# Kernel optimization log

Hardware: AMD Instinct MI355X
Metric: run time of the kernel (lower is better)

The kernel has to match this reference:

```python
import jax, jax.numpy as jnp
import numpy as np

NEG_SLOPE = 0.2  # PyG GATConv default negative_slope


def gat_conv(x, src, dst, W, a_src, a_dst, b, n_nodes):
    # x: [N, Cin]; W: [H, Cin, Cout]; a_src/a_dst: [H, Cout]; b: [Cout]
    xh = jnp.einsum('ni,hio->nho', x, W)                 # [N, H, Cout]
    al_s = jnp.einsum('nho,ho->nh', xh, a_src)           # [N, H]
    al_d = jnp.einsum('nho,ho->nh', xh, a_dst)           # [N, H]
    e = jax.nn.leaky_relu(al_s[src] + al_d[dst], NEG_SLOPE)  # [E, H]
    # softmax over incoming edges of each dst node (self-loops guarantee >=1 edge)
    m = jax.ops.segment_max(e, dst, num_segments=n_nodes)
    ex = jnp.exp(e - m[dst])
    den = jax.ops.segment_sum(ex, dst, num_segments=n_nodes)
    alpha = ex / den[dst]                                # [E, H]
    msg = alpha[:, :, None] * xh[src]                    # [E, H, Cout]
    out = jax.ops.segment_sum(msg, dst, num_segments=n_nodes)  # [N, H, Cout]
    return out.mean(axis=1) + b                          # concat=False -> head mean


def setup_inputs() -> dict:
    key = jax.random.key(0)
    ks = jax.random.split(key, 16)
    N, E, C, H = 20000, 320000, 128, 4
    s = 1.0 / np.sqrt(C)
    inp = {
        'x': jax.random.normal(ks[0], (N, C), dtype=jnp.float32),
        'edge_index': jax.random.randint(ks[1], (2, E), 0, N, dtype=jnp.int64),
    }
    for i, name in enumerate(['1', '2', 'r']):
        k0, k1, k2 = jax.random.split(ks[2 + i], 3)
        inp['W' + name] = jax.random.normal(k0, (H, C, C), dtype=jnp.float32) * s
        inp['as' + name] = jax.random.normal(k1, (H, C), dtype=jnp.float32) * s
        inp['ad' + name] = jax.random.normal(k2, (H, C), dtype=jnp.float32) * s
        inp['b' + name] = jnp.zeros((C,), dtype=jnp.float32)
    return inp


def reference(x, edge_index, W1, as1, ad1, b1, W2, as2, ad2, b2, Wr, asr, adr, br):
    n = x.shape[0]
    loop = jnp.arange(n, dtype=edge_index.dtype)
    src = jnp.concatenate([edge_index[0], loop])  # PyG add_self_loops=True
    dst = jnp.concatenate([edge_index[1], loop])
    h = gat_conv(x, src, dst, W1, as1, ad1, b1, n)
    h = gat_conv(h, src, dst, W2, as2, ad2, b2, n)
    res = gat_conv(x, src, dst, Wr, asr, adr, br, n)
    return h + res
```

## Files before the change

### kernel.cpp

```cpp
#include <hip/hip_runtime.h>
#include <math.h>

#define C 128

typedef unsigned short u16;
typedef __attribute__((ext_vector_type(8))) short short8;
typedef __attribute__((ext_vector_type(4))) float f32x4;
typedef __attribute__((ext_vector_type(4))) u16 u16x4;

__device__ __forceinline__ float b2f(u16 u) {
    union { unsigned i; float f; } x; x.i = (unsigned)u << 16; return x.f;
}
__device__ __forceinline__ u16 f2b(float f) {
    union { float f; unsigned i; } x; x.f = f;
    unsigned r = x.i + 0x7FFFu + ((x.i >> 16) & 1u);
    return (u16)(r >> 16);
}
__device__ __forceinline__ float lrelu(float x) { return x > 0.f ? x : 0.2f * x; }


__global__ void hist_kernel(const int* __restrict__ ei, int E, int N,
                            int* __restrict__ count) {
    int total = E + N;
    for (int e = blockIdx.x * blockDim.x + threadIdx.x; e < total;
         e += gridDim.x * blockDim.x) {
        int d = (e < E) ? ei[E + e] : (e - E);
        if ((unsigned)d < (unsigned)N) atomicAdd(&count[d], 1);
    }
}

__global__ __launch_bounds__(1024) void scan_kernel(const int* __restrict__ count,
                                                    int* __restrict__ offs,
                                                    int* __restrict__ cursor, int N) {
    int tid = threadIdx.x, lane = tid & 63, wid = tid >> 6;
    int CH = (N + 1023) >> 10;
    int base = tid * CH;
    int s = 0;
    for (int j = 0; j < CH; ++j) {
        int i = base + j;
        if (i < N) s += count[i];
    }
    int own = s;
    #pragma unroll
    for (int d = 1; d < 64; d <<= 1) {
        int v = __shfl_up(s, d);
        if (lane >= d) s += v;
    }
    __shared__ int wtot[16];
    if (lane == 63) wtot[wid] = s;
    __syncthreads();
    if (tid < 16) {
        int t = wtot[tid];
        int u = t;
        #pragma unroll
        for (int d = 1; d < 16; d <<= 1) {
            int v = __shfl_up(u, d);
            if (tid >= d) u += v;
        }
        wtot[tid] = u - t;
        if (tid == 15) offs[N] = u;
    }
    __syncthreads();
    int run = wtot[wid] + s - own;
    for (int j = 0; j < CH; ++j) {
        int i = base + j;
        if (i < N) {
            offs[i] = run;
            cursor[i] = run;
            run += count[i];
        }
    }
}

__global__ void scatter_kernel(const int* __restrict__ ei, int E, int N,
                               int* __restrict__ cursor, int* __restrict__ srcs,
                               int* __restrict__ dsts) {
    int total = E + N;
    for (int e = blockIdx.x * blockDim.x + threadIdx.x; e < total;
         e += gridDim.x * blockDim.x) {
        int sNode, d;
        if (e < E) { sNode = ei[e]; d = ei[E + e]; }
        else       { sNode = e - E; d = sNode; }
        if ((unsigned)d < (unsigned)N && (unsigned)sNode < (unsigned)N) {
            int pos = atomicAdd(&cursor[d], 1);
            srcs[pos] = sNode;
            dsts[pos] = d;
        }
    }
}


__global__ __launch_bounds__(256) void cvt_w_kernel(const float* __restrict__ W1,
                                                    const float* __restrict__ Wr,
                                                    const float* __restrict__ W2,
                                                    u16* __restrict__ Wf) {
    int idx = blockIdx.x * 256 + threadIdx.x;
    int lane = idx & 63;
    int kk = (idx >> 6) & 15;
    int t = (idx >> 10) & 7;
    int l = idx >> 13;
    if (l >= 3) return;
    const float* W = (l == 0) ? W1 : (l == 1) ? Wr : W2;
    int o = t * 16 + (lane & 15);
    int bk = kk * 32 + (lane >> 4) * 8;
    int h = bk >> 7, i0 = bk & 127;
    short8 v;
    #pragma unroll
    for (int j = 0; j < 8; ++j) {
        v[j] = (short)f2b(0.25f * W[((size_t)h * C + i0 + j) * C + o]);
    }
    *(short8*)(Wf + (size_t)idx * 8) = v;
}


__global__ __launch_bounds__(256) void wvec_kernel(const float* __restrict__ W1,
                                                   const float* __restrict__ as1,
                                                   const float* __restrict__ ad1,
                                                   const float* __restrict__ Wr,
                                                   const float* __restrict__ asr,
                                                   const float* __restrict__ adr,
                                                   const float* __restrict__ W2,
                                                   const float* __restrict__ as2,
                                                   const float* __restrict__ ad2,
                                                   u16* __restrict__ vsdA,
                                                   u16* __restrict__ vsdB) {
    int slot = blockIdx.x;
    const float* W  = (slot < 4) ? W1 : (slot < 8) ? Wr : W2;
    const float* s_ = (slot < 4) ? as1 : (slot < 8) ? asr : as2;
    const float* d_ = (slot < 4) ? ad1 : (slot < 8) ? adr : ad2;
    int h = slot & 3;
    int wave = threadIdx.x >> 6, lane = threadIdx.x & 63;
    int rbase = blockIdx.y * 32 + wave * 8;
    float as0 = s_[h * C + lane], as1v = s_[h * C + 64 + lane];
    float ad0 = d_[h * C + lane], ad1v = d_[h * C + 64 + lane];
    #pragma unroll
    for (int j = 0; j < 8; ++j) {
        int i = rbase + j;
        const float* Wrow = W + ((size_t)h * C + i) * C;
        float w0 = Wrow[lane], w1 = Wrow[64 + lane];
        float ps = w0 * as0 + w1 * as1v;
        float pd = w0 * ad0 + w1 * ad1v;
        #pragma unroll
        for (int m = 32; m; m >>= 1) {
            ps += __shfl_xor(ps, m);
            pd += __shfl_xor(pd, m);
        }
        if (lane == 0) {
            if (slot < 8) {
                vsdA[slot * C + i] = f2b(ps);
                vsdA[(8 + slot) * C + i] = f2b(pd);
            } else {
                vsdB[(slot - 8) * C + i] = f2b(ps);
                vsdB[(4 + (slot - 8)) * C + i] = f2b(pd);
            }
        }
    }
}


__global__ __launch_bounds__(256) void alA_kernel(const float* __restrict__ x,
                                                  const u16* __restrict__ vsd,
                                                  u16* __restrict__ xb,
                                                  float* __restrict__ als,
                                                  float* __restrict__ ald, int N) {
    int wave = threadIdx.x >> 6, lane = threadIdx.x & 63;
    int rowBase = blockIdx.x * 64 + wave * 16;
    int r = rowBase + (lane & 15);
    int rl = r < N ? r : N - 1;
    int kg = (lane >> 4) * 8;

    short8 a[4];
    #pragma unroll
    for (int t = 0; t < 4; ++t) {
        const float* xp = x + (size_t)rl * C + t * 32 + kg;
        float4 f0 = *(const float4*)xp;
        float4 f1 = *(const float4*)(xp + 4);
        short8 s;
        s[0] = f2b(f0.x); s[1] = f2b(f0.y); s[2] = f2b(f0.z); s[3] = f2b(f0.w);
        s[4] = f2b(f1.x); s[5] = f2b(f1.y); s[6] = f2b(f1.z); s[7] = f2b(f1.w);
        a[t] = s;
        if (r < N) *(short8*)(xb + (size_t)r * C + t * 32 + kg) = s;
    }
    f32x4 acc = {0.f, 0.f, 0.f, 0.f};
    int col = lane & 15;
    #pragma unroll
    for (int t = 0; t < 4; ++t) {
        short8 b = *(const short8*)(vsd + (size_t)col * C + t * 32 + kg);
        acc = __builtin_amdgcn_mfma_f32_16x16x32_bf16(a[t], b, acc, 0, 0, 0);
    }
    #pragma unroll
    for (int j = 0; j < 4; ++j) {
        int rr = rowBase + (lane >> 4) * 4 + j;
        if (rr < N) {
            if (col < 8) als[rr * 8 + col] = acc[j];
            else ald[rr * 8 + (col - 8)] = acc[j];
        }
    }
}


__global__ __launch_bounds__(256) void alB_kernel(const u16* __restrict__ in,
                                                  const u16* __restrict__ vsd,
                                                  float* __restrict__ als,
                                                  float* __restrict__ ald, int N) {
    int wave = threadIdx.x >> 6, lane = threadIdx.x & 63;
    int rowBase = blockIdx.x * 64 + wave * 16;
    int r = rowBase + (lane & 15);
    int rl = r < N ? r : N - 1;
    int kg = (lane >> 4) * 8;

    f32x4 acc = {0.f, 0.f, 0.f, 0.f};
    int col = lane & 15;
    #pragma unroll
    for (int t = 0; t < 4; ++t) {
        short8 a = *(const short8*)(in + (size_t)rl * C + t * 32 + kg);
        short8 b = *(const short8*)(vsd + (size_t)col * C + t * 32 + kg);
        acc = __builtin_amdgcn_mfma_f32_16x16x32_bf16(a, b, acc, 0, 0, 0);
    }
    #pragma unroll
    for (int j = 0; j < 4; ++j) {
        int rr = rowBase + (lane >> 4) * 4 + j;
        if (rr < N && col < 8) {
            if (col < 4) als[rr * 4 + col] = acc[j];
            else ald[rr * 4 + (col - 4)] = acc[j];
        }
    }
}


template <int NH>
__global__ __launch_bounds__(256) void ew_kernel(const float* __restrict__ als,
                                                 const float* __restrict__ ald,
                                                 const int* __restrict__ srcs,
                                                 const int* __restrict__ dsts,
                                                 float* __restrict__ wout, int ET) {
    int i = blockIdx.x * blockDim.x + threadIdx.x;
    if (i >= ET) return;
    int s = srcs[i], d = dsts[i];
    const float* as_ = als + (size_t)s * NH;
    const float* ad_ = ald + (size_t)d * NH;
    float* wo = wout + (size_t)i * NH;
    #pragma unroll
    for (int h = 0; h < NH; ++h) {
        wo[h] = __expf(lrelu(as_[h] + ad_[h]));
    }
}


template <int NH>
__global__ __launch_bounds__(256) void den_kernel(const float* __restrict__ wgt,
                                                  const int* __restrict__ offs,
                                                  float* __restrict__ den, int N) {
    int idx = blockIdx.x * blockDim.x + threadIdx.x;
    int node = idx / NH, h = idx % NH;
    if (node >= N) return;
    int beg = offs[node], end = offs[node + 1];
    float s = 0.f;
    for (int i = beg; i < end; ++i) s += wgt[(size_t)i * NH + h];
    den[idx] = s;
}


template <int NH>
__global__ __launch_bounds__(256) void aggx_kernel(const u16* __restrict__ xsrc,
                                                   const float* __restrict__ wgt,
                                                   const float* __restrict__ den,
                                                   const int* __restrict__ offs,
                                                   const int* __restrict__ srcs,
                                                   u16* __restrict__ dest, int N) {
    constexpr int NHG = NH / 2;
    int node = blockIdx.x * 4 + (threadIdx.x >> 6);
    int lane = threadIdx.x & 63;
    if (node >= N) return;
    int g = lane >> 5;
    int c0 = (lane & 31) * 4;
    int beg = offs[node], end = offs[node + 1];

    float inv[NHG];
    #pragma unroll
    for (int j = 0; j < NHG; ++j) {
        inv[j] = 1.f / den[(size_t)node * NH + g * NHG + j];
    }

    float acc[NHG][4] = {};
    int i = beg;
    for (; i + 8 <= end; i += 8) {
        int s[8];
        #pragma unroll
        for (int e = 0; e < 8; ++e) s[e] = srcs[i + e];
        u16x4 v[8];
        #pragma unroll
        for (int e = 0; e < 8; ++e) {
            v[e] = *(const u16x4*)(xsrc + (size_t)s[e] * C + c0);
        }
        float wv[8][NHG];
        #pragma unroll
        for (int e = 0; e < 8; ++e) {
            if constexpr (NHG == 4) {
                float4 wq = *(const float4*)(wgt + (size_t)(i + e) * NH + g * NHG);
                wv[e][0] = wq.x; wv[e][1] = wq.y; wv[e][2] = wq.z; wv[e][3] = wq.w;
            } else {
                float2 wq = *(const float2*)(wgt + (size_t)(i + e) * NH + g * NHG);
                wv[e][0] = wq.x; wv[e][1] = wq.y;
            }
        }
        #pragma unroll
        for (int e = 0; e < 8; ++e) {
            float f[4];
            #pragma unroll
            for (int j = 0; j < 4; ++j) f[j] = b2f(v[e][j]);
            #pragma unroll
            for (int j2 = 0; j2 < NHG; ++j2) {
                #pragma unroll
                for (int j = 0; j < 4; ++j) acc[j2][j] += wv[e][j2] * f[j];
            }
        }
    }
    for (; i < end; ++i) {
        int s0 = srcs[i];
        u16x4 v0 = *(const u16x4*)(xsrc + (size_t)s0 * C + c0);
        float w0[NHG];
        #pragma unroll
        for (int j2 = 0; j2 < NHG; ++j2) {
            w0[j2] = wgt[(size_t)i * NH + g * NHG + j2];
        }
        float f[4];
        #pragma unroll
        for (int j = 0; j < 4; ++j) f[j] = b2f(v0[j]);
        #pragma unroll
        for (int j2 = 0; j2 < NHG; ++j2) {
            #pragma unroll
            for (int j = 0; j < 4; ++j) acc[j2][j] += w0[j2] * f[j];
        }
    }

    #pragma unroll
    for (int j2 = 0; j2 < NHG; ++j2) {
        int h = g * NHG + j2;
        u16x4 o = {f2b(acc[j2][0] * inv[j2]), f2b(acc[j2][1] * inv[j2]),
                   f2b(acc[j2][2] * inv[j2]), f2b(acc[j2][3] * inv[j2])};
        *(u16x4*)(dest + (size_t)node * (NH * C) + h * C + c0) = o;
    }
}


__global__ __launch_bounds__(256) void gemm2ab_kernel(const u16* __restrict__ agg,
                                                      const u16* __restrict__ Wf,
                                                      const float* __restrict__ b1,
                                                      const float* __restrict__ br,
                                                      u16* __restrict__ h1b,
                                                      float* __restrict__ outf, int N) {
    int part = blockIdx.y;
    const float* bias = part ? br : b1;
    int wave = threadIdx.x >> 6, lane = threadIdx.x & 63;
    int rowBase = blockIdx.x * 128 + wave * 32;
    int p = lane & 15, q = lane >> 4;
    int r0 = rowBase + p, r1 = rowBase + 16 + p;
    int rl0 = r0 < N ? r0 : N - 1;
    int rl1 = r1 < N ? r1 : N - 1;
    int kg = q * 8;

    const short8* ap0 = (const short8*)(agg + (size_t)rl0 * 1024 + part * 512 + kg);
    const short8* ap1 = (const short8*)(agg + (size_t)rl1 * 1024 + part * 512 + kg);
    const u16* wb = Wf + (size_t)part * 65536 + lane * 8;

    f32x4 acc0[8], acc1[8];
    #pragma unroll
    for (int t = 0; t < 8; ++t) {
        acc0[t] = (f32x4){0.f, 0.f, 0.f, 0.f};
        acc1[t] = (f32x4){0.f, 0.f, 0.f, 0.f};
    }

    #pragma unroll
    for (int kk = 0; kk < 16; ++kk) {
        short8 a0 = ap0[kk * 4];
        short8 a1 = ap1[kk * 4];
        #pragma unroll
        for (int t = 0; t < 8; ++t) {
            short8 b = *(const short8*)(wb + (size_t)(t * 16 + kk) * 512);
            acc0[t] = __builtin_amdgcn_mfma_f32_16x16x32_bf16(a0, b, acc0[t], 0, 0, 0);
            acc1[t] = __builtin_amdgcn_mfma_f32_16x16x32_bf16(a1, b, acc1[t], 0, 0, 0);
        }
    }

    #pragma unroll
    for (int t = 0; t < 8; ++t) {
        int col = t * 16 + p;
        float bcol = bias[col];
        #pragma unroll
        for (int j = 0; j < 4; ++j) {
            int rr0 = rowBase + q * 4 + j;
            int rr1 = rowBase + 16 + q * 4 + j;
            if (rr0 < N) {
                float v = acc0[t][j] + bcol;
                if (part == 0) h1b[(size_t)rr0 * C + col] = f2b(v);
                else outf[(size_t)rr0 * C + col] = v;
            }
            if (rr1 < N) {
                float v = acc1[t][j] + bcol;
                if (part == 0) h1b[(size_t)rr1 * C + col] = f2b(v);
                else outf[(size_t)rr1 * C + col] = v;
            }
        }
    }
}


__global__ __launch_bounds__(256) void gemm2c_kernel(const u16* __restrict__ A,
                                                     const u16* __restrict__ Wf,
                                                     const float* __restrict__ bias,
                                                     float* __restrict__ outf, int N) {
    int wave = threadIdx.x >> 6, lane = threadIdx.x & 63;
    int rowBase = blockIdx.x * 128 + wave * 32;
    int p = lane & 15, q = lane >> 4;
    int r0 = rowBase + p, r1 = rowBase + 16 + p;
    int rl0 = r0 < N ? r0 : N - 1;
    int rl1 = r1 < N ? r1 : N - 1;
    int kg = q * 8;

    const short8* ap0 = (const short8*)(A + (size_t)rl0 * 512 + kg);
    const short8* ap1 = (const short8*)(A + (size_t)rl1 * 512 + kg);
    const u16* wb = Wf + (size_t)2 * 65536 + lane * 8;

    f32x4 acc0[8], acc1[8];
    #pragma unroll
    for (int t = 0; t < 8; ++t) {
        acc0[t] = (f32x4){0.f, 0.f, 0.f, 0.f};
        acc1[t] = (f32x4){0.f, 0.f, 0.f, 0.f};
    }

    #pragma unroll
    for (int kk = 0; kk < 16; ++kk) {
        short8 a0 = ap0[kk * 4];
        short8 a1 = ap1[kk * 4];
        #pragma unroll
        for (int t = 0; t < 8; ++t) {
            short8 b = *(const short8*)(wb + (size_t)(t * 16 + kk) * 512);
            acc0[t] = __builtin_amdgcn_mfma_f32_16x16x32_bf16(a0, b, acc0[t], 0, 0, 0);
            acc1[t] = __builtin_amdgcn_mfma_f32_16x16x32_bf16(a1, b, acc1[t], 0, 0, 0);
        }
    }

    #pragma unroll
    for (int t = 0; t < 8; ++t) {
        int col = t * 16 + p;
        float bcol = bias[col];
        #pragma unroll
        for (int j = 0; j < 4; ++j) {
            int rr0 = rowBase + q * 4 + j;
            int rr1 = rowBase + 16 + q * 4 + j;
            if (rr0 < N) outf[(size_t)rr0 * C + col] += acc0[t][j] + bcol;
            if (rr1 < N) outf[(size_t)rr1 * C + col] += acc1[t][j] + bcol;
        }
    }
}


extern "C" void kernel_launch(void* const* d_in, const int* in_sizes, int n_in,
                              void* d_out, int out_size, void* d_ws, size_t ws_size,
                              hipStream_t stream) {
    const float* x = (const float*)d_in[0];
    const int* ei = (const int*)d_in[1];
    const float* W1 = (const float*)d_in[2];
    const float* as1 = (const float*)d_in[3];
    const float* ad1 = (const float*)d_in[4];
    const float* b1 = (const float*)d_in[5];
    const float* W2 = (const float*)d_in[6];
    const float* as2 = (const float*)d_in[7];
    const float* ad2 = (const float*)d_in[8];
    const float* b2 = (const float*)d_in[9];
    const float* Wr = (const float*)d_in[10];
    const float* asr = (const float*)d_in[11];
    const float* adr = (const float*)d_in[12];
    const float* br = (const float*)d_in[13];

    int N = in_sizes[0] / C;
    int E = in_sizes[1] / 2;
    int ET = E + N;

    size_t sz_xb    = (size_t)N * C * 2;
    size_t sz_h1b   = (size_t)N * C * 2;
    size_t sz_aggA  = (size_t)N * 1024 * 2;
    size_t sz_aggB  = (size_t)N * 512 * 2;
    size_t sz_wc    = (size_t)3 * C * 512 * 2;
    size_t sz_vsd   = (size_t)16 * C * 2;
    size_t sz_al8   = (size_t)N * 8 * 4;
    size_t sz_count = (size_t)N * 4;
    size_t sz_den8  = (size_t)N * 8 * 4;
    size_t sz_den4  = (size_t)N * 4 * 4;
    size_t sz_offs  = (size_t)(N + 4) * 4;
    size_t sz_srcs  = (size_t)ET * 4;
    size_t sz_w     = (size_t)ET * 8 * 4;
    size_t required = sz_xb + sz_h1b + sz_aggA + sz_aggB + sz_wc + 2 * sz_vsd +
                      2 * sz_al8 + sz_count + sz_den8 + sz_den4 + sz_count +
                      sz_offs + 2 * sz_srcs + sz_w;
    if (ws_size < required) return;

    char* w = (char*)d_ws;
    u16* xb = (u16*)w;        w += sz_xb;
    u16* h1b = (u16*)w;       w += sz_h1b;
    u16* aggA = (u16*)w;      w += sz_aggA;
    u16* aggB = (u16*)w;      w += sz_aggB;
    u16* Wf = (u16*)w;        w += sz_wc;
    u16* vsdA = (u16*)w;      w += sz_vsd;
    u16* vsdB = (u16*)w;      w += sz_vsd;
    float* als = (float*)w;   w += sz_al8;
    float* ald = (float*)w;   w += sz_al8;
    int* count = (int*)w;     w += sz_count;
    float* den8 = (float*)w;  w += sz_den8;
    float* den4 = (float*)w;  w += sz_den4;
    int* cursor = (int*)w;    w += sz_count;
    int* offs = (int*)w;      w += sz_offs;
    int* srcs = (int*)w;      w += sz_srcs;
    int* dsts = (int*)w;      w += sz_srcs;
    float* wgt = (float*)w;   w += sz_w;
    float* out = (float*)d_out;

    hipMemsetAsync(count, 0, sz_count, stream);
    hist_kernel<<<512, 256, 0, stream>>>(ei, E, N, count);
    scan_kernel<<<1, 1024, 0, stream>>>(count, offs, cursor, N);
    scatter_kernel<<<512, 256, 0, stream>>>(ei, E, N, cursor, srcs, dsts);

    cvt_w_kernel<<<96, 256, 0, stream>>>(W1, Wr, W2, Wf);
    wvec_kernel<<<dim3(12, 4), 256, 0, stream>>>(W1, as1, ad1, Wr, asr, adr,
                                                 W2, as2, ad2, vsdA, vsdB);

    int nwb = (N + 3) / 4;
    int neb = (ET + 255) / 256;
    int gx = (N + 63) / 64;
    int gx2 = (N + 127) / 128;
    int nd8 = (N * 8 + 255) / 256;
    int nd4 = (N * 4 + 255) / 256;

    alA_kernel<<<gx, 256, 0, stream>>>(x, vsdA, xb, als, ald, N);
    ew_kernel<8><<<neb, 256, 0, stream>>>(als, ald, srcs, dsts, wgt, ET);
    den_kernel<8><<<nd8, 256, 0, stream>>>(wgt, offs, den8, N);
    aggx_kernel<8><<<nwb, 256, 0, stream>>>(xb, wgt, den8, offs, srcs, aggA, N);
    gemm2ab_kernel<<<dim3(gx2, 2), 256, 0, stream>>>(aggA, Wf, b1, br, h1b, out, N);

    alB_kernel<<<gx, 256, 0, stream>>>(h1b, vsdB, als, ald, N);
    ew_kernel<4><<<neb, 256, 0, stream>>>(als, ald, srcs, dsts, wgt, ET);
    den_kernel<4><<<nd4, 256, 0, stream>>>(wgt, offs, den4, N);
    aggx_kernel<4><<<nwb, 256, 0, stream>>>(h1b, wgt, den4, offs, srcs, aggB, N);
    gemm2c_kernel<<<gx2, 256, 0, stream>>>(aggB, Wf, b2, out, N);
}
```

Before: 365.9 us.

## Fuse edge-weight computation into denominator kernel and merge residual GEMM into final GEMM

The separate per-edge exp kernel is folded into the per-node denominator kernel, which now computes and stores the edge weights while summing them. This removes the dsts array and one edge-wide pass. The residual-branch GEMM moves from the layer-1 GEMM into the final GEMM, which accumulates both products and writes the output once instead of read-modify-write. The GEMMs now use 64-row tiles with a 2-way column split for more blocks. Per-node serial edge loops in the denominator kernel may load-balance worse than the old per-edge kernel.

```diff
diff --git a/kernel.cpp b/kernel.cpp
--- a/kernel.cpp
+++ b/kernel.cpp
@@ -73,8 +73,7 @@
 }
 
 __global__ void scatter_kernel(const int* __restrict__ ei, int E, int N,
-                               int* __restrict__ cursor, int* __restrict__ srcs,
-                               int* __restrict__ dsts) {
+                               int* __restrict__ cursor, int* __restrict__ srcs) {
     int total = E + N;
     for (int e = blockIdx.x * blockDim.x + threadIdx.x; e < total;
          e += gridDim.x * blockDim.x) {
@@ -84,7 +83,6 @@
         if ((unsigned)d < (unsigned)N && (unsigned)sNode < (unsigned)N) {
             int pos = atomicAdd(&cursor[d], 1);
             srcs[pos] = sNode;
-            dsts[pos] = d;
         }
     }
 }
@@ -229,34 +227,23 @@
 
 
 template <int NH>
-__global__ __launch_bounds__(256) void ew_kernel(const float* __restrict__ als,
-                                                 const float* __restrict__ ald,
-                                                 const int* __restrict__ srcs,
-                                                 const int* __restrict__ dsts,
-                                                 float* __restrict__ wout, int ET) {
-    int i = blockIdx.x * blockDim.x + threadIdx.x;
-    if (i >= ET) return;
-    int s = srcs[i], d = dsts[i];
-    const float* as_ = als + (size_t)s * NH;
-    const float* ad_ = ald + (size_t)d * NH;
-    float* wo = wout + (size_t)i * NH;
-    #pragma unroll
-    for (int h = 0; h < NH; ++h) {
-        wo[h] = __expf(lrelu(as_[h] + ad_[h]));
-    }
-}
-
-
-template <int NH>
-__global__ __launch_bounds__(256) void den_kernel(const float* __restrict__ wgt,
-                                                  const int* __restrict__ offs,
-                                                  float* __restrict__ den, int N) {
+__global__ __launch_bounds__(256) void denf_kernel(const float* __restrict__ als,
+                                                   const float* __restrict__ ald,
+                                                   const int* __restrict__ offs,
+                                                   const int* __restrict__ srcs,
+                                                   float* __restrict__ wgt,
+                                                   float* __restrict__ den, int N) {
     int idx = blockIdx.x * blockDim.x + threadIdx.x;
     int node = idx / NH, h = idx % NH;
     if (node >= N) return;
+    float adh = ald[(size_t)node * NH + h];
     int beg = offs[node], end = offs[node + 1];
     float s = 0.f;
-    for (int i = beg; i < end; ++i) s += wgt[(size_t)i * NH + h];
+    for (int i = beg; i < end; ++i) {
+        float w = __expf(lrelu(als[(size_t)srcs[i] * NH + h] + adh));
+        wgt[(size_t)i * NH + h] = w;
+        s += w;
+    }
     den[idx] = s;
 }
 
@@ -344,113 +331,98 @@
 }
 
 
-__global__ __launch_bounds__(256) void gemm2ab_kernel(const u16* __restrict__ agg,
-                                                      const u16* __restrict__ Wf,
-                                                      const float* __restrict__ b1,
-                                                      const float* __restrict__ br,
-                                                      u16* __restrict__ h1b,
-                                                      float* __restrict__ outf, int N) {
-    int part = blockIdx.y;
-    const float* bias = part ? br : b1;
+__global__ __launch_bounds__(256) void gemmL1_kernel(const u16* __restrict__ agg,
+                                                     const u16* __restrict__ Wf,
+                                                     const float* __restrict__ b1,
+                                                     u16* __restrict__ h1b, int N) {
     int wave = threadIdx.x >> 6, lane = threadIdx.x & 63;
-    int rowBase = blockIdx.x * 128 + wave * 32;
+    int ch = blockIdx.y;
+    int rowBase = blockIdx.x * 64 + wave * 16;
     int p = lane & 15, q = lane >> 4;
-    int r0 = rowBase + p, r1 = rowBase + 16 + p;
-    int rl0 = r0 < N ? r0 : N - 1;
-    int rl1 = r1 < N ? r1 : N - 1;
+    int r = rowBase + p;
+    int rl = r < N ? r : N - 1;
     int kg = q * 8;
 
-    const short8* ap0 = (const short8*)(agg + (size_t)rl0 * 1024 + part * 512 + kg);
-    const short8* ap1 = (const short8*)(agg + (size_t)rl1 * 1024 + part * 512 + kg);
-    const u16* wb = Wf + (size_t)part * 65536 + lane * 8;
-
-    f32x4 acc0[8], acc1[8];
-    #pragma unroll
-    for (int t = 0; t < 8; ++t) {
-        acc0[t] = (f32x4){0.f, 0.f, 0.f, 0.f};
-        acc1[t] = (f32x4){0.f, 0.f, 0.f, 0.f};
-    }
+    const short8* ap = (const short8*)(agg + (size_t)rl * 1024 + kg);
+    const u16* wb = Wf + (size_t)(ch * 4 * 16) * 512 + lane * 8;
+
+    f32x4 acc[4];
+    #pragma unroll
+    for (int t = 0; t < 4; ++t) acc[t] = (f32x4){0.f, 0.f, 0.f, 0.f};
 
     #pragma unroll
     for (int kk = 0; kk < 16; ++kk) {
-        short8 a0 = ap0[kk * 4];
-        short8 a1 = ap1[kk * 4];
-        #pragma unroll
-        for (int t = 0; t < 8; ++t) {
+        short8 a = ap[kk * 4];
+        #pragma unroll
+        for (int t = 0; t < 4; ++t) {
             short8 b = *(const short8*)(wb + (size_t)(t * 16 + kk) * 512);
-            acc0[t] = __builtin_amdgcn_mfma_f32_16x16x32_bf16(a0, b, acc0[t], 0, 0, 0);
-            acc1[t] = __builtin_amdgcn_mfma_f32_16x16x32_bf16(a1, b, acc1[t], 0, 0, 0);
-        }
-    }
-
-    #pragma unroll
-    for (int t = 0; t < 8; ++t) {
-        int col = t * 16 + p;
-        float bcol = bias[col];
+            acc[t] = __builtin_amdgcn_mfma_f32_16x16x32_bf16(a, b, acc[t], 0, 0, 0);
+        }
+    }
+
+    #pragma unroll
+    for (int t = 0; t < 4; ++t) {
+        int col = (ch * 4 + t) * 16 + p;
+        float bcol = b1[col];
         #pragma unroll
         for (int j = 0; j < 4; ++j) {
-            int rr0 = rowBase + q * 4 + j;
-            int rr1 = rowBase + 16 + q * 4 + j;
-            if (rr0 < N) {
-                float v = acc0[t][j] + bcol;
-                if (part == 0) h1b[(size_t)rr0 * C + col] = f2b(v);
-                else outf[(size_t)rr0 * C + col] = v;
-            }
-            if (rr1 < N) {
-                float v = acc1[t][j] + bcol;
-                if (part == 0) h1b[(size_t)rr1 * C + col] = f2b(v);
-                else outf[(size_t)rr1 * C + col] = v;
-            }
-        }
-    }
-}
-
-
-__global__ __launch_bounds__(256) void gemm2c_kernel(const u16* __restrict__ A,
-                                                     const u16* __restrict__ Wf,
-                                                     const float* __restrict__ bias,
-                                                     float* __restrict__ outf, int N) {
+            int rr = rowBase + q * 4 + j;
+            if (rr < N) h1b[(size_t)rr * C + col] = f2b(acc[t][j] + bcol);
+        }
+    }
+}
+
+
+__global__ __launch_bounds__(256) void gemmF_kernel(const u16* __restrict__ aggB,
+                                                    const u16* __restrict__ aggA,
+                                                    const u16* __restrict__ Wf,
+                                                    const float* __restrict__ b2,
+                                                    const float* __restrict__ br,
+                                                    float* __restrict__ outf, int N) {
     int wave = threadIdx.x >> 6, lane = threadIdx.x & 63;
-    int rowBase = blockIdx.x * 128 + wave * 32;
+    int ch = blockIdx.y;
+    int rowBase = blockIdx.x * 64 + wave * 16;
     int p = lane & 15, q = lane >> 4;
-    int r0 = rowBase + p, r1 = rowBase + 16 + p;
-    int rl0 = r0 < N ? r0 : N - 1;
-    int rl1 = r1 < N ? r1 : N - 1;
+    int r = rowBase + p;
+    int rl = r < N ? r : N - 1;
     int kg = q * 8;
 
-    const short8* ap0 = (const short8*)(A + (size_t)rl0 * 512 + kg);
-    const short8* ap1 = (const short8*)(A + (size_t)rl1 * 512 + kg);
-    const u16* wb = Wf + (size_t)2 * 65536 + lane * 8;
-
-    f32x4 acc0[8], acc1[8];
-    #pragma unroll
-    for (int t = 0; t < 8; ++t) {
-        acc0[t] = (f32x4){0.f, 0.f, 0.f, 0.f};
-        acc1[t] = (f32x4){0.f, 0.f, 0.f, 0.f};
-    }
+    const short8* apB = (const short8*)(aggB + (size_t)rl * 512 + kg);
+    const short8* apR = (const short8*)(aggA + (size_t)rl * 1024 + 512 + kg);
+    const u16* wb2 = Wf + (size_t)2 * 65536 + (size_t)(ch * 4 * 16) * 512 + lane * 8;
+    const u16* wbr = Wf + (size_t)1 * 65536 + (size_t)(ch * 4 * 16) * 512 + lane * 8;
+
+    f32x4 acc[4];
+    #pragma unroll
+    for (int t = 0; t < 4; ++t) acc[t] = (f32x4){0.f, 0.f, 0.f, 0.f};
 
     #pragma unroll
     for (int kk = 0; kk < 16; ++kk) {
-        short8 a0 = ap0[kk * 4];
-        short8 a1 = ap1[kk * 4];
-        #pragma unroll
-        for (int t = 0; t < 8; ++t) {
-            short8 b = *(const short8*)(wb + (size_t)(t * 16 + kk) * 512);
-            acc0[t] = __builtin_amdgcn_mfma_f32_16x16x32_bf16(a0, b, acc0[t], 0, 0, 0);
-            acc1[t] = __builtin_amdgcn_mfma_f32_16x16x32_bf16(a1, b, acc1[t], 0, 0, 0);
-        }
-    }
-
-    #pragma unroll
-    for (int t = 0; t < 8; ++t) {
-        int col = t * 16 + p;
-        float bcol = bias[col];
+        short8 a = apB[kk * 4];
+        #pragma unroll
+        for (int t = 0; t < 4; ++t) {
+            short8 b = *(const short8*)(wb2 + (size_t)(t * 16 + kk) * 512);
+            acc[t] = __builtin_amdgcn_mfma_f32_16x16x32_bf16(a, b, acc[t], 0, 0, 0);
+        }
+    }
+    #pragma unroll
+    for (int kk = 0; kk < 16; ++kk) {
+        short8 a = apR[kk * 4];
+        #pragma unroll
+        for (int t = 0; t < 4; ++t) {
+            short8 b = *(const short8*)(wbr + (size_t)(t * 16 + kk) * 512);
+            acc[t] = __builtin_amdgcn_mfma_f32_16x16x32_bf16(a, b, acc[t], 0, 0, 0);
+        }
+    }
+
+    #pragma unroll
+    for (int t = 0; t < 4; ++t) {
+        int col = (ch * 4 + t) * 16 + p;
+        float bcol = b2[col] + br[col];
         #pragma unroll
         for (int j = 0; j < 4; ++j) {
-            int rr0 = rowBase + q * 4 + j;
-            int rr1 = rowBase + 16 + q * 4 + j;
-            if (rr0 < N) outf[(size_t)rr0 * C + col] += acc0[t][j] + bcol;
-            if (rr1 < N) outf[(size_t)rr1 * C + col] += acc1[t][j] + bcol;
+            int rr = rowBase + q * 4 + j;
+            if (rr < N) outf[(size_t)rr * C + col] = acc[t][j] + bcol;
         }
     }
 }
@@ -512,35 +484,31 @@
     int* cursor = (int*)w;    w += sz_count;
     int* offs = (int*)w;      w += sz_offs;
     int* srcs = (int*)w;      w += sz_srcs;
-    int* dsts = (int*)w;      w += sz_srcs;
+    w += sz_srcs;
     float* wgt = (float*)w;   w += sz_w;
     float* out = (float*)d_out;
 
     hipMemsetAsync(count, 0, sz_count, stream);
     hist_kernel<<<512, 256, 0, stream>>>(ei, E, N, count);
     scan_kernel<<<1, 1024, 0, stream>>>(count, offs, cursor, N);
-    scatter_kernel<<<512, 256, 0, stream>>>(ei, E, N, cursor, srcs, dsts);
+    scatter_kernel<<<512, 256, 0, stream>>>(ei, E, N, cursor, srcs);
 
     cvt_w_kernel<<<96, 256, 0, stream>>>(W1, Wr, W2, Wf);
     wvec_kernel<<<dim3(12, 4), 256, 0, stream>>>(W1, as1, ad1, Wr, asr, adr,
                                                  W2, as2, ad2, vsdA, vsdB);
 
     int nwb = (N + 3) / 4;
-    int neb = (ET + 255) / 256;
     int gx = (N + 63) / 64;
-    int gx2 = (N + 127) / 128;
     int nd8 = (N * 8 + 255) / 256;
     int nd4 = (N * 4 + 255) / 256;
 
     alA_kernel<<<gx, 256, 0, stream>>>(x, vsdA, xb, als, ald, N);
-    ew_kernel<8><<<neb, 256, 0, stream>>>(als, ald, srcs, dsts, wgt, ET);
-    den_kernel<8><<<nd8, 256, 0, stream>>>(wgt, offs, den8, N);
+    denf_kernel<8><<<nd8, 256, 0, stream>>>(als, ald, offs, srcs, wgt, den8, N);
     aggx_kernel<8><<<nwb, 256, 0, stream>>>(xb, wgt, den8, offs, srcs, aggA, N);
-    gemm2ab_kernel<<<dim3(gx2, 2), 256, 0, stream>>>(aggA, Wf, b1, br, h1b, out, N);
+    gemmL1_kernel<<<dim3(gx, 2), 256, 0, stream>>>(aggA, Wf, b1, h1b, N);
 
     alB_kernel<<<gx, 256, 0, stream>>>(h1b, vsdB, als, ald, N);
-    ew_kernel<4><<<neb, 256, 0, stream>>>(als, ald, srcs, dsts, wgt, ET);
-    den_kernel<4><<<nd4, 256, 0, stream>>>(wgt, offs, den4, N);
+    denf_kernel<4><<<nd4, 256, 0, stream>>>(als, ald, offs, srcs, wgt, den4, N);
     aggx_kernel<4><<<nwb, 256, 0, stream>>>(h1b, wgt, den4, offs, srcs, aggB, N);
-    gemm2c_kernel<<<gx2, 256, 0, stream>>>(aggB, Wf, b2, out, N);
-}
+    gemmF_kernel<<<dim3(gx, 2), 256, 0, stream>>>(aggB, aggA, Wf, b2, br, out, N);
+}
```

After: 309.0 us. 1.18x faster.
